# Kernel tuning notes

Measured on AMD Instinct MI355X. Metric: run time of the kernel, lower is better.

## Reference

```python
import jax, jax.numpy as jnp
import numpy as np

DIM = 1536
NHEADS = 12
HDIM = DIM // NHEADS  # 128
EPS = 1e-6
LOCAL_ATTN_SIZE = 3
SINK_SIZE = 1
MAX_ATTN = 32760 if LOCAL_ATTN_SIZE == -1 else LOCAL_ATTN_SIZE * 1560  # 4680


def _rms(x, g):
    # WanRMSNorm over last dim
    return x * jax.lax.rsqrt(jnp.mean(x * x, axis=-1, keepdims=True) + EPS) * g


def _rope(x, f, h, w, fr, fi, start_frame):
    # x: [b, s, n, d] with s == f*h*w; fr/fi: [1024, d//2] real/imag of complex rotations
    b, s, n, d = x.shape
    c = d // 2
    c0 = c - 2 * (c // 3)
    c1 = c // 3
    fc = jax.lax.complex(fr, fi)  # [1024, c]
    xr = x.reshape(b, s, n, c, 2)
    xc = jax.lax.complex(xr[..., 0], xr[..., 1])  # [b, s, n, c]
    ff = fc[start_frame:start_frame + f, :c0]      # [f, c0]
    fh = fc[:h, c0:c0 + c1]                        # [h, c1]
    fw = fc[:w, c0 + c1:c0 + 2 * c1]               # [w, c1]
    freqs_i = jnp.concatenate([
        jnp.broadcast_to(ff[:, None, None, :], (f, h, w, c0)),
        jnp.broadcast_to(fh[None, :, None, :], (f, h, w, c1)),
        jnp.broadcast_to(fw[None, None, :, :], (f, h, w, c1)),
    ], axis=-1).reshape(1, s, 1, c)
    y = xc * freqs_i
    return jnp.stack([y.real, y.imag], axis=-1).reshape(b, s, n, d)


def _attn(q, k, v):
    # plain SDPA (decode path of the module uses no mask on the gathered window)
    scale = 1.0 / np.sqrt(q.shape[-1]).astype(np.float32)
    logits = jnp.einsum('bqnd,bknd->bnqk', q, k) * scale
    p = jax.nn.softmax(logits, axis=-1)
    return jnp.einsum('bnqk,bknd->bqnd', p, v)


def _forward(x, cache_k, cache_v, freqs_real, freqs_imag,
             wq, bq, wk, bk, wv, bv, wo, bo, gq, gk,
             f_frames, height, width, current_start, global_end_index, local_end_index):
    b, s, _ = x.shape
    n, d = NHEADS, HDIM
    frame_seqlen = height * width
    start_frame = current_start // frame_seqlen

    q = _rms(x @ wq + bq, gq).reshape(b, s, n, d)
    k = _rms(x @ wk + bk, gk).reshape(b, s, n, d)
    v = (x @ wv + bv).reshape(b, s, n, d)

    rq = _rope(q, f_frames, height, width, freqs_real, freqs_imag, start_frame)
    rk = _rope(k, f_frames, height, width, freqs_real, freqs_imag, start_frame)

    current_end = current_start + s
    sink_tokens = SINK_SIZE * frame_seqlen
    kv_size = cache_k.shape[1]
    is_recompute = (current_end <= global_end_index) and (current_start > 0)

    kc, vc = cache_k, cache_v
    if LOCAL_ATTN_SIZE != -1 and current_end > global_end_index and s + local_end_index > kv_size:
        # evict oldest non-sink tokens, roll the rest toward the sink region
        num_evicted = s + local_end_index - kv_size
        num_rolled = local_end_index - num_evicted - sink_tokens
        src = slice(sink_tokens + num_evicted, sink_tokens + num_evicted + num_rolled)
        kc = kc.at[:, sink_tokens:sink_tokens + num_rolled].set(jax.lax.stop_gradient(cache_k[:, src]))
        vc = vc.at[:, sink_tokens:sink_tokens + num_rolled].set(jax.lax.stop_gradient(cache_v[:, src]))
        new_local_end = local_end_index + current_end - global_end_index - num_evicted
    else:
        new_local_end = local_end_index + current_end - global_end_index
    local_start = new_local_end - s
    write_start = max(local_start, sink_tokens) if is_recompute else local_start
    off = max(0, write_start - local_start)
    wl = max(0, new_local_end - write_start)
    if wl > 0:
        kc = kc.at[:, write_start:new_local_end].set(rk[:, off:off + wl])
        vc = vc.at[:, write_start:new_local_end].set(v[:, off:off + wl])

    if sink_tokens > 0:
        budget = MAX_ATTN - sink_tokens
        if budget > 0:
            lo = max(sink_tokens, new_local_end - budget)
            kcat = jnp.concatenate([kc[:, :sink_tokens], kc[:, lo:new_local_end]], axis=1)
            vcat = jnp.concatenate([vc[:, :sink_tokens], vc[:, lo:new_local_end]], axis=1)
        else:
            kcat, vcat = kc[:, :sink_tokens], vc[:, :sink_tokens]
        o = _attn(rq, kcat, vcat)
    else:
        ws = max(0, new_local_end - MAX_ATTN)
        o = _attn(rq, kc[:, ws:new_local_end], vc[:, ws:new_local_end])

    return o.reshape(b, s, DIM) @ wo + bo


def setup_inputs() -> dict:
    key = jax.random.key(0)
    ks = jax.random.split(key, 12)
    B, S, CACHE = 1, 1560, 4680
    sc = 0.02
    # RoPE tables as unit-magnitude complex rotations
    ang = jax.random.uniform(ks[0], (1024, HDIM // 2), jnp.float32, 0.0, 2.0 * np.pi)
    return {
        'x': jax.random.normal(ks[1], (B, S, DIM), jnp.float32),
        'cache_k': jax.random.normal(ks[2], (B, CACHE, NHEADS, HDIM), jnp.float32),
        'cache_v': jax.random.normal(ks[3], (B, CACHE, NHEADS, HDIM), jnp.float32),
        'freqs_real': jnp.cos(ang),
        'freqs_imag': jnp.sin(ang),
        'wq': jax.random.normal(ks[4], (DIM, DIM), jnp.float32) * sc,
        'bq': jnp.zeros((DIM,), jnp.float32),
        'wk': jax.random.normal(ks[5], (DIM, DIM), jnp.float32) * sc,
        'bk': jnp.zeros((DIM,), jnp.float32),
        'wv': jax.random.normal(ks[6], (DIM, DIM), jnp.float32) * sc,
        'bv': jnp.zeros((DIM,), jnp.float32),
        'wo': jax.random.normal(ks[7], (DIM, DIM), jnp.float32) * sc,
        'bo': jnp.zeros((DIM,), jnp.float32),
        'gq': jnp.ones((DIM,), jnp.float32),
        'gk': jnp.ones((DIM,), jnp.float32),
        'f_frames': 1,
        'height': 30,
        'width': 52,
        'current_start': 4680,
        'global_end_index': 4680,
        'local_end_index': 4680,
    }


def reference(x, cache_k, cache_v, freqs_real, freqs_imag,
              wq, bq, wk, bk, wv, bv, wo, bo, gq, gk,
              f_frames, height, width, current_start, global_end_index, local_end_index):
    return _forward(x, cache_k, cache_v, freqs_real, freqs_imag,
                    wq, bq, wk, bk, wv, bv, wo, bo, gq, gk,
                    f_frames, height, width, current_start, global_end_index, local_end_index)
```

## Files before the change

### kernel.cpp

```cpp
#include <hip/hip_runtime.h>
#include <cstdint>
#include <cstddef>

typedef unsigned int  u32;
typedef unsigned short u16;
typedef short s16x8 __attribute__((ext_vector_type(8)));
typedef float f32x4 __attribute__((ext_vector_type(4)));

#define DIM     1536
#define NH      12
#define HD      128
#define SEQ     1560
#define MPAD    1664
#define NKV     4680
#define NKPAD   4736
#define ROLL0   3120
#define NQK     4608
#define START_FRAME 3
#define NEGINF  -3.0e4f
#define NSPLIT  4
#define SPLITKC 1216

__device__ __forceinline__ u16 f2bf(float f){
  u32 u = __builtin_bit_cast(u32, f);
  u32 r = (u + 0x7fffu + ((u >> 16) & 1u)) >> 16;
  return (u16)r;
}

__global__ void k_pre(const float* __restrict__ x, u16* __restrict__ xp,
                      u16* __restrict__ Kc, u16* __restrict__ VT,
                      u16* __restrict__ Qr, u16* __restrict__ Opad,
                      float* __restrict__ sumsq,
                      const float* __restrict__ ck, const float* __restrict__ cv,
                      const float* __restrict__ wq, const float* __restrict__ wk,
                      const float* __restrict__ wv, const float* __restrict__ wo,
                      u16* __restrict__ WTqkv, u16* __restrict__ WTo){
  __shared__ u32 tile[64][65];
  int b = blockIdx.x, t = threadIdx.x;
  if (b < 244){
    int i = b * 256 + t;
    uint4 z = make_uint4(0u, 0u, 0u, 0u);
    if (i < 10752){
      int h = i / 896, r = i % 896;
      ((uint4*)(Kc + ((size_t)h * NKPAD + NKV) * 128))[r] = z;
    } else if (i < 21504){
      int j = i - 10752; int row = j / 7, c = j % 7;
      ((uint4*)(VT + (size_t)row * NKPAD + NKV))[c] = z;
    } else if (i < 41472){
      int j = i - 21504; int h = j / 1664, r = j % 1664;
      ((uint4*)(Qr + ((size_t)h * MPAD + SEQ) * 128))[r] = z;
    } else if (i < 61440){
      int r = i - 41472;
      ((uint4*)(Opad + (size_t)SEQ * DIM))[r] = z;
    } else if (i < 62272){
      ((uint4*)sumsq)[i - 61440] = z;
    }
  } else if (b < 1492){
    int i = (b - 244) * 256 + t;
    const int n_src = SEQ * DIM / 8;
    u16 o[8] = {0,0,0,0,0,0,0,0};
    if (i < n_src){
      float4 a = ((const float4*)x)[2*i];
      float4 c = ((const float4*)x)[2*i + 1];
      o[0]=f2bf(a.x); o[1]=f2bf(a.y); o[2]=f2bf(a.z); o[3]=f2bf(a.w);
      o[4]=f2bf(c.x); o[5]=f2bf(c.y); o[6]=f2bf(c.z); o[7]=f2bf(c.w);
    }
    uint4 v = make_uint4((u32)o[0]|((u32)o[1]<<16), (u32)o[2]|((u32)o[3]<<16),
                         (u32)o[4]|((u32)o[5]<<16), (u32)o[6]|((u32)o[7]<<16));
    ((uint4*)xp)[i] = v;
  } else if (b < 3832){
    int i = (b - 1492) * 256 + t;
    int p = i / 192, j = i - p * 192;
    int src = (p < SEQ) ? p : p + SEQ;
    int h = j >> 4, d = (j & 15) * 8;
    const float* s = ck + (size_t)src * DIM + j * 8;
    float4 a = ((const float4*)s)[0], bb = ((const float4*)s)[1];
    uint4 v = make_uint4((u32)f2bf(a.x)|((u32)f2bf(a.y)<<16), (u32)f2bf(a.z)|((u32)f2bf(a.w)<<16),
                         (u32)f2bf(bb.x)|((u32)f2bf(bb.y)<<16), (u32)f2bf(bb.z)|((u32)f2bf(bb.w)<<16));
    *(uint4*)(Kc + (size_t)(h * NKPAD + p) * 128 + d) = v;
  } else if (b < 5008){
    int idx = b - 3832;
    int p0 = (idx % 49) * 64, hd0 = (idx / 49) * 64;
    int pr = t >> 4, cg = t & 15;
#pragma unroll
    for (int i = 0; i < 4; i++){
      int p = p0 + pr + i * 16;
      if (p < ROLL0){
        int src = (p < SEQ) ? p : p + SEQ;
        float4 v = *(const float4*)(cv + (size_t)src * DIM + hd0 + cg * 4);
        tile[pr + i*16][cg*4+0] = f2bf(v.x); tile[pr + i*16][cg*4+1] = f2bf(v.y);
        tile[pr + i*16][cg*4+2] = f2bf(v.z); tile[pr + i*16][cg*4+3] = f2bf(v.w);
      }
    }
    __syncthreads();
    int hd = t >> 2, pg = t & 3;
    int pbase = p0 + pg * 16;
    if (pbase < ROLL0){
      u32 wds[8];
#pragma unroll
      for (int j = 0; j < 8; j++)
        wds[j] = (tile[pg*16 + 2*j][hd] & 0xffffu) | (tile[pg*16 + 2*j + 1][hd] << 16);
      u16* q = VT + (size_t)(hd0 + hd) * NKPAD + pbase;
      *(uint4*)q       = make_uint4(wds[0], wds[1], wds[2], wds[3]);
      *(uint4*)(q + 8) = make_uint4(wds[4], wds[5], wds[6], wds[7]);
    }
  } else {
    int idx = b - 5008;
    int z = idx / 576, rem = idx % 576;
    const float* w = (z==0)?wq:(z==1)?wk:(z==2)?wv:wo;
    u16* dst = (z < 3) ? (WTqkv + (size_t)z * DIM * DIM) : WTo;
    int r0 = (rem % 24) * 64, c0 = (rem / 24) * 64;
    int rr = t >> 4, cg = t & 15;
#pragma unroll
    for (int i = 0; i < 4; i++){
      int r = rr + i * 16;
      float4 v = *(const float4*)(w + (size_t)(r0 + r) * DIM + c0 + cg * 4);
      tile[r][cg*4+0] = f2bf(v.x); tile[r][cg*4+1] = f2bf(v.y);
      tile[r][cg*4+2] = f2bf(v.z); tile[r][cg*4+3] = f2bf(v.w);
    }
    __syncthreads();
    int c = t >> 2, rg = t & 3;
    u32 wds[8];
#pragma unroll
    for (int j = 0; j < 8; j++)
      wds[j] = (tile[rg*16 + 2*j][c] & 0xffffu) | (tile[rg*16 + 2*j + 1][c] << 16);
    u16* q = dst + (size_t)(c0 + c) * DIM + r0 + rg * 16;
    *(uint4*)q       = make_uint4(wds[0], wds[1], wds[2], wds[3]);
    *(uint4*)(q + 8) = make_uint4(wds[4], wds[5], wds[6], wds[7]);
  }
}

#define LDK 40
__global__ __launch_bounds__(512) void k_gemm_qkv(
    const u16* __restrict__ A, const u16* __restrict__ B,
    const float* __restrict__ biasq, const float* __restrict__ biask, const float* __restrict__ biasv,
    float* __restrict__ Y, float* __restrict__ sumsq, u16* __restrict__ VT){
  __shared__ u16 As[128*LDK];
  __shared__ u16 Bs[256*LDK];
  int orig = blockIdx.y * 18 + blockIdx.x;
  int xcd = orig & 7, jj = orig >> 3;
  int wg = (xcd < 2 ? xcd * 30 : 60 + (xcd - 2) * 29) + jj;
  int n0 = (wg % 18) * 256;
  int m0 = (wg / 18) * 128;
  int t = threadIdx.x, w = t >> 6, lane = t & 63, quad = lane >> 4, lc = lane & 15;
  int wm = w & 1, wn = w >> 1;
  int ar = t >> 2, ac = (t & 3) * 8;
  int br = t >> 1, bc = (t & 1) * 16;
  f32x4 acc[4][4] = {};
  uint4 pa, pb0, pb1;
  {
    pa = *(const uint4*)(A + (size_t)(m0 + ar) * DIM + ac);
    const uint4* gb = (const uint4*)(B + (size_t)(n0 + br) * DIM + bc);
    pb0 = gb[0]; pb1 = gb[1];
  }
  for (int kt = 0; kt < DIM/32; kt++){
    __syncthreads();
    *(uint4*)(As + ar * LDK + ac)     = pa;
    *(uint4*)(Bs + br * LDK + bc)     = pb0;
    *(uint4*)(Bs + br * LDK + bc + 8) = pb1;
    __syncthreads();
    if (kt + 1 < DIM/32){
      int k0 = (kt + 1) * 32;
      pa = *(const uint4*)(A + (size_t)(m0 + ar) * DIM + k0 + ac);
      const uint4* gb = (const uint4*)(B + (size_t)(n0 + br) * DIM + k0 + bc);
      pb0 = gb[0]; pb1 = gb[1];
    }
    s16x8 af[4], bf[4];
#pragma unroll
    for (int mt = 0; mt < 4; mt++) af[mt] = *(const s16x8*)(As + (wm*64 + mt*16 + lc) * LDK + quad * 8);
#pragma unroll
    for (int nt = 0; nt < 4; nt++) bf[nt] = *(const s16x8*)(Bs + (wn*64 + nt*16 + lc) * LDK + quad * 8);
#pragma unroll
    for (int mt = 0; mt < 4; mt++)
#pragma unroll
      for (int nt = 0; nt < 4; nt++)
        acc[mt][nt] = __builtin_amdgcn_mfma_f32_16x16x32_bf16(af[mt], bf[nt], acc[mt][nt], 0, 0, 0);
  }
  const float* bias; int cbase; int which;
  if (n0 < DIM)        { bias = biasq; cbase = 0;     which = 0; }
  else if (n0 < 2*DIM) { bias = biask; cbase = DIM;   which = 1; }
  else                 { bias = biasv; cbase = 2*DIM; which = 2; }
  float bvals[4];
#pragma unroll
  for (int nt = 0; nt < 4; nt++) bvals[nt] = bias[n0 - cbase + wn*64 + nt*16 + lc];
  if (which == 2){
#pragma unroll
    for (int mt = 0; mt < 4; mt++){
      int row0 = m0 + wm*64 + mt*16 + quad*4;
      if (row0 < SEQ){
#pragma unroll
        for (int nt = 0; nt < 4; nt++){
          int hd = (n0 - 2*DIM) + wn*64 + nt*16 + lc;
          u32 lo = (u32)f2bf(acc[mt][nt][0] + bvals[nt]) | ((u32)f2bf(acc[mt][nt][1] + bvals[nt]) << 16);
          u32 hi = (u32)f2bf(acc[mt][nt][2] + bvals[nt]) | ((u32)f2bf(acc[mt][nt][3] + bvals[nt]) << 16);
          *(uint2*)(VT + (size_t)hd * NKPAD + ROLL0 + row0) = make_uint2(lo, hi);
        }
      }
    }
  } else {
#pragma unroll
    for (int mt = 0; mt < 4; mt++){
      int row0 = m0 + wm*64 + mt*16 + quad*4;
      float ss[4] = {0.f, 0.f, 0.f, 0.f};
#pragma unroll
      for (int nt = 0; nt < 4; nt++){
        int col = n0 + wn*64 + nt*16 + lc;
#pragma unroll
        for (int r = 0; r < 4; r++){
          float y = acc[mt][nt][r] + bvals[nt];
          Y[(size_t)(row0 + r) * NQK + col] = y;
          ss[r] += y * y;
        }
      }
      float* dst = sumsq + (which ? MPAD : 0);
#pragma unroll
      for (int r = 0; r < 4; r++){
        float v = ss[r];
        v += __shfl_xor(v, 1); v += __shfl_xor(v, 2); v += __shfl_xor(v, 4); v += __shfl_xor(v, 8);
        if (lc == 0) atomicAdd(&dst[row0 + r], v);
      }
    }
  }
}

__global__ void k_rope_qk(const float* __restrict__ Y, const float* __restrict__ sumsq,
                          const float* __restrict__ gq, const float* __restrict__ gk,
                          const float* __restrict__ fre, const float* __restrict__ fim,
                          u16* __restrict__ Qr, u16* __restrict__ Kc){
  int pos = blockIdx.x;
  int t = threadIdx.x;
  float scq = rsqrtf(sumsq[pos]        * (1.0f/1536.0f) + 1e-6f);
  float sck = rsqrtf(sumsq[MPAD + pos] * (1.0f/1536.0f) + 1e-6f);
  int hrow = pos / 52, wrow = pos % 52;
#pragma unroll
  for (int i = 0; i < 3; i++){
    int p = t + i * 256;
    int head = p >> 6, j = p & 63;
    int frow = (j < 22) ? START_FRAME : ((j < 43) ? hrow : wrow);
    float cr = fre[frow * 64 + j], ci = fim[frow * 64 + j];
    int d0 = head * 128 + 2 * j;
    float2 yq = *(const float2*)(Y + (size_t)pos * NQK + d0);
    float qa = yq.x * scq * gq[d0];
    float qb = yq.y * scq * gq[d0 + 1];
    u32 oq = (u32)f2bf(qa * cr - qb * ci) | ((u32)f2bf(qa * ci + qb * cr) << 16);
    *(u32*)(Qr + (size_t)(head * MPAD + pos) * 128 + 2 * j) = oq;
    float2 yk = *(const float2*)(Y + (size_t)pos * NQK + DIM + d0);
    float ka = yk.x * sck * gk[d0];
    float kb = yk.y * sck * gk[d0 + 1];
    u32 ok = (u32)f2bf(ka * cr - kb * ci) | ((u32)f2bf(ka * ci + kb * cr) << 16);
    *(u32*)(Kc + (size_t)(head * NKPAD + ROLL0 + pos) * 128 + 2 * j) = ok;
  }
}

#define DEFER_THR 8.0f
__global__ __launch_bounds__(512, 4) void k_attn(const u16* __restrict__ Qr, const u16* __restrict__ Kc,
                                                 const u16* __restrict__ VT,
                                                 float* __restrict__ Opart, float* __restrict__ ml){
  __shared__ u16 Ks[64 * 128];
  __shared__ u16 Vs[128 * 64];
  int h = blockIdx.y, qb = blockIdx.x, sp = blockIdx.z;
  int t = threadIdx.x, w = t >> 6, lane = t & 63, quad = lane >> 4, lc = lane & 15;
  int qbase = qb * 128 + w * 16;
  const u16* Qbase = Qr + (size_t)(h * MPAD + qbase + lc) * 128;
  s16x8 qf[4];
#pragma unroll
  for (int kk = 0; kk < 4; kk++) qf[kk] = *(const s16x8*)(Qbase + kk * 32 + quad * 8);
  f32x4 oacc[8] = {};
  float m_ = NEGINF;
  float l_ = 0.f;
  const float scale = 0.08838834764831845f;
  const u16* Kh = Kc + (size_t)h * NKPAD * 128;
  const u16* Vh = VT + (size_t)h * 128 * NKPAD;
  int kr0 = t >> 4,          kg0 = (t & 15) * 8;
  int kr1 = (t + 512) >> 4,  kg1 = ((t + 512) & 15) * 8;
  int vd0 = t >> 3,          vp0 = (t & 7) * 8;
  int vd1 = (t + 512) >> 3,  vp1 = ((t + 512) & 7) * 8;
  int ksw0 = kr0 * 128 + (kg0 ^ ((kr0 & 7) << 3));
  int ksw1 = kr1 * 128 + (kg1 ^ ((kr1 & 7) << 3));
  int vsw0 = vd0 * 64  + (vp0 ^ ((vd0 & 7) << 3));
  int vsw1 = vd1 * 64  + (vp1 ^ ((vd1 & 7) << 3));
  int xork = (lc & 7) << 3;
  int aa = (lc + ((quad & 1) << 5)) << 2;
  int ab = aa + 64;
  int hi = quad >> 1;

  int kc0 = sp * SPLITKC;
  int kc1 = (sp == NSPLIT-1) ? NKPAD : kc0 + SPLITKC;
  uint4 kp0, kp1, vq0, vq1;
  {
    int kc = kc0;
    kp0 = *(const uint4*)(Kh + (size_t)(kc + kr0) * 128 + kg0);
    kp1 = *(const uint4*)(Kh + (size_t)(kc + kr1) * 128 + kg1);
    vq0 = *(const uint4*)(Vh + (size_t)vd0 * NKPAD + kc + vp0);
    vq1 = *(const uint4*)(Vh + (size_t)vd1 * NKPAD + kc + vp1);
  }
  for (int kc = kc0; kc < kc1; kc += 64){
    __syncthreads();
    *(uint4*)(Ks + ksw0) = kp0;
    *(uint4*)(Ks + ksw1) = kp1;
    *(uint4*)(Vs + vsw0) = vq0;
    *(uint4*)(Vs + vsw1) = vq1;
    __syncthreads();
    if (kc + 64 < kc1){
      int kn = kc + 64;
      kp0 = *(const uint4*)(Kh + (size_t)(kn + kr0) * 128 + kg0);
      kp1 = *(const uint4*)(Kh + (size_t)(kn + kr1) * 128 + kg1);
      vq0 = *(const uint4*)(Vh + (size_t)vd0 * NKPAD + kn + vp0);
      vq1 = *(const uint4*)(Vh + (size_t)vd1 * NKPAD + kn + vp1);
    }
    float s[4][4];
    __builtin_amdgcn_s_setprio(1);
#pragma unroll
    for (int nt = 0; nt < 4; nt++){
      f32x4 acc = {};
      int p = nt * 16 + lc;
#pragma unroll
      for (int kk = 0; kk < 4; kk++){
        s16x8 kf = *(const s16x8*)(Ks + p * 128 + (((kk * 4 + quad) * 8) ^ xork));
        acc = __builtin_amdgcn_mfma_f32_16x16x32_bf16(kf, qf[kk], acc, 0, 0, 0);
      }
#pragma unroll
      for (int r = 0; r < 4; r++) s[nt][r] = acc[r] * scale;
    }
    __builtin_amdgcn_s_setprio(0);
    if (kc + 64 > NKV){
#pragma unroll
      for (int nt = 0; nt < 4; nt++){
        int keyb = kc + nt * 16 + quad * 4;
#pragma unroll
        for (int r = 0; r < 4; r++) if (keyb + r >= NKV) s[nt][r] = NEGINF;
      }
    }
    float mx = fmaxf(fmaxf(s[0][0], s[0][1]), fmaxf(s[0][2], s[0][3]));
#pragma unroll
    for (int nt = 1; nt < 4; nt++)
      mx = fmaxf(mx, fmaxf(fmaxf(s[nt][0], s[nt][1]), fmaxf(s[nt][2], s[nt][3])));
    mx = fmaxf(mx, __shfl_xor(mx, 16));
    mx = fmaxf(mx, __shfl_xor(mx, 32));
    if (__any(mx > m_ + DEFER_THR)){
      float mnew = fmaxf(m_, mx);
      float alpha = __expf(m_ - mnew);
      m_ = mnew; l_ *= alpha;
      float alr[4];
#pragma unroll
      for (int r = 0; r < 4; r++) alr[r] = __shfl(alpha, quad * 4 + r);
#pragma unroll
      for (int dt = 0; dt < 8; dt++){
        f32x4 oo = oacc[dt];
#pragma unroll
        for (int r = 0; r < 4; r++) oo[r] *= alr[r];
        oacc[dt] = oo;
      }
    }
#pragma unroll
    for (int nt = 0; nt < 4; nt++)
#pragma unroll
      for (int r = 0; r < 4; r++) s[nt][r] = __expf(s[nt][r] - m_);
    float sum = (s[0][0] + s[0][1]) + (s[0][2] + s[0][3]);
#pragma unroll
    for (int nt = 1; nt < 4; nt++)
      sum += (s[nt][0] + s[nt][1]) + (s[nt][2] + s[nt][3]);
    sum += __shfl_xor(sum, 16);
    sum += __shfl_xor(sum, 32);
    l_ += sum;
    u32 w01[4], w23[4];
#pragma unroll
    for (int nt = 0; nt < 4; nt++){
      w01[nt] = (u32)f2bf(s[nt][0]) | ((u32)f2bf(s[nt][1]) << 16);
      w23[nt] = (u32)f2bf(s[nt][2]) | ((u32)f2bf(s[nt][3]) << 16);
    }
    u32 x0, x1;
    uint4 A0, A1;
    x0 = (u32)__builtin_amdgcn_ds_bpermute(aa, (int)w01[0]);
    x1 = (u32)__builtin_amdgcn_ds_bpermute(aa, (int)w01[1]);
    A0.x = hi ? x1 : x0;
    x0 = (u32)__builtin_amdgcn_ds_bpermute(aa, (int)w23[0]);
    x1 = (u32)__builtin_amdgcn_ds_bpermute(aa, (int)w23[1]);
    A0.y = hi ? x1 : x0;
    x0 = (u32)__builtin_amdgcn_ds_bpermute(ab, (int)w01[0]);
    x1 = (u32)__builtin_amdgcn_ds_bpermute(ab, (int)w01[1]);
    A0.z = hi ? x1 : x0;
    x0 = (u32)__builtin_amdgcn_ds_bpermute(ab, (int)w23[0]);
    x1 = (u32)__builtin_amdgcn_ds_bpermute(ab, (int)w23[1]);
    A0.w = hi ? x1 : x0;
    x0 = (u32)__builtin_amdgcn_ds_bpermute(aa, (int)w01[2]);
    x1 = (u32)__builtin_amdgcn_ds_bpermute(aa, (int)w01[3]);
    A1.x = hi ? x1 : x0;
    x0 = (u32)__builtin_amdgcn_ds_bpermute(aa, (int)w23[2]);
    x1 = (u32)__builtin_amdgcn_ds_bpermute(aa, (int)w23[3]);
    A1.y = hi ? x1 : x0;
    x0 = (u32)__builtin_amdgcn_ds_bpermute(ab, (int)w01[2]);
    x1 = (u32)__builtin_amdgcn_ds_bpermute(ab, (int)w01[3]);
    A1.z = hi ? x1 : x0;
    x0 = (u32)__builtin_amdgcn_ds_bpermute(ab, (int)w23[2]);
    x1 = (u32)__builtin_amdgcn_ds_bpermute(ab, (int)w23[3]);
    A1.w = hi ? x1 : x0;
    s16x8 a0 = __builtin_bit_cast(s16x8, A0);
    s16x8 a1 = __builtin_bit_cast(s16x8, A1);
    __builtin_amdgcn_s_setprio(1);
#pragma unroll
    for (int dt = 0; dt < 8; dt++){
      int d = dt * 16 + lc;
      s16x8 v0 = *(const s16x8*)(Vs + d * 64 + ((quad * 8) ^ xork));
      s16x8 v1 = *(const s16x8*)(Vs + d * 64 + ((32 + quad * 8) ^ xork));
      oacc[dt] = __builtin_amdgcn_mfma_f32_16x16x32_bf16(a0, v0, oacc[dt], 0, 0, 0);
      oacc[dt] = __builtin_amdgcn_mfma_f32_16x16x32_bf16(a1, v1, oacc[dt], 0, 0, 0);
    }
    __builtin_amdgcn_s_setprio(0);
  }
  float mr[4], lr[4];
#pragma unroll
  for (int r = 0; r < 4; r++){
    mr[r] = __shfl(m_, quad * 4 + r);
    lr[r] = __shfl(l_, quad * 4 + r);
  }
  float* Ob = Opart + ((size_t)(sp * NH + h) * SEQ) * 128;
  float* mlb = ml + ((size_t)(sp * NH + h) * SEQ) * 2;
#pragma unroll
  for (int dt = 0; dt < 8; dt++)
#pragma unroll
    for (int r = 0; r < 4; r++){
      int row = qbase + quad * 4 + r;
      if (row < SEQ) Ob[(size_t)row * 128 + dt * 16 + lc] = oacc[dt][r];
    }
  if (lc == 0){
#pragma unroll
    for (int r = 0; r < 4; r++){
      int row = qbase + quad * 4 + r;
      if (row < SEQ){
        mlb[row * 2 + 0] = mr[r];
        mlb[row * 2 + 1] = lr[r];
      }
    }
  }
}

__global__ void k_attn_cmb(const float* __restrict__ Opart, const float* __restrict__ ml,
                           u16* __restrict__ Og){
  int row = blockIdx.x, h = blockIdx.y, d = threadIdx.x;
  float m[NSPLIT], l[NSPLIT];
  float M = NEGINF;
#pragma unroll
  for (int s = 0; s < NSPLIT; s++){
    m[s] = ml[((size_t)(s * NH + h) * SEQ + row) * 2 + 0];
    l[s] = ml[((size_t)(s * NH + h) * SEQ + row) * 2 + 1];
    M = fmaxf(M, m[s]);
  }
  float L = 0.f, o = 0.f;
#pragma unroll
  for (int s = 0; s < NSPLIT; s++){
    float wgt = __expf(m[s] - M);
    L += wgt * l[s];
    o += wgt * Opart[((size_t)(s * NH + h) * SEQ + row) * 128 + d];
  }
  Og[(size_t)row * DIM + h * 128 + d] = f2bf(o / L);
}

__global__ __launch_bounds__(256) void k_gemm_out(const u16* __restrict__ A, const u16* __restrict__ B,
                                                  const float* __restrict__ bo, float* __restrict__ out){
  __shared__ u16 As[128*LDK];
  __shared__ u16 Bs[128*LDK];
  int m0 = blockIdx.y * 128, n0 = blockIdx.x * 128;
  int t = threadIdx.x, w = t >> 6, lane = t & 63, quad = lane >> 4, lc = lane & 15;
  int wm = w & 1, wn = w >> 1;
  int sr = t >> 1, sh = (t & 1) * 16;
  f32x4 acc[4][4] = {};
  uint4 pa0, pa1, pb0, pb1;
  {
    const uint4* ga = (const uint4*)(A + (size_t)(m0 + sr) * DIM + sh);
    const uint4* gb = (const uint4*)(B + (size_t)(n0 + sr) * DIM + sh);
    pa0 = ga[0]; pa1 = ga[1]; pb0 = gb[0]; pb1 = gb[1];
  }
  for (int kt = 0; kt < DIM/32; kt++){
    __syncthreads();
    *(uint4*)(As + sr * LDK + sh)     = pa0;
    *(uint4*)(As + sr * LDK + sh + 8) = pa1;
    *(uint4*)(Bs + sr * LDK + sh)     = pb0;
    *(uint4*)(Bs + sr * LDK + sh + 8) = pb1;
    __syncthreads();
    if (kt + 1 < DIM/32){
      int k0 = (kt + 1) * 32;
      const uint4* ga = (const uint4*)(A + (size_t)(m0 + sr) * DIM + k0 + sh);
      const uint4* gb = (const uint4*)(B + (size_t)(n0 + sr) * DIM + k0 + sh);
      pa0 = ga[0]; pa1 = ga[1]; pb0 = gb[0]; pb1 = gb[1];
    }
    s16x8 af[4], bf[4];
#pragma unroll
    for (int mt = 0; mt < 4; mt++) af[mt] = *(const s16x8*)(As + (wm*64 + mt*16 + lc) * LDK + quad * 8);
#pragma unroll
    for (int nt = 0; nt < 4; nt++) bf[nt] = *(const s16x8*)(Bs + (wn*64 + nt*16 + lc) * LDK + quad * 8);
#pragma unroll
    for (int mt = 0; mt < 4; mt++)
#pragma unroll
      for (int nt = 0; nt < 4; nt++)
        acc[mt][nt] = __builtin_amdgcn_mfma_f32_16x16x32_bf16(af[mt], bf[nt], acc[mt][nt], 0, 0, 0);
  }
  float bvals[4];
#pragma unroll
  for (int nt = 0; nt < 4; nt++) bvals[nt] = bo[n0 + wn*64 + nt*16 + lc];
#pragma unroll
  for (int mt = 0; mt < 4; mt++){
    int row0 = m0 + wm*64 + mt*16 + quad*4;
#pragma unroll
    for (int nt = 0; nt < 4; nt++){
      int col = n0 + wn*64 + nt*16 + lc;
#pragma unroll
      for (int r = 0; r < 4; r++){
        int row = row0 + r;
        if (row < SEQ) out[(size_t)row * DIM + col] = acc[mt][nt][r] + bvals[nt];
      }
    }
  }
}

extern "C" void kernel_launch(void* const* d_in, const int* in_sizes, int n_in,
                              void* d_out, int out_size, void* d_ws, size_t ws_size,
                              hipStream_t stream){
  const float* x   = (const float*)d_in[0];
  const float* ck  = (const float*)d_in[1];
  const float* cv  = (const float*)d_in[2];
  const float* fre = (const float*)d_in[3];
  const float* fim = (const float*)d_in[4];
  const float* wq  = (const float*)d_in[5];
  const float* bq  = (const float*)d_in[6];
  const float* wk  = (const float*)d_in[7];
  const float* bk  = (const float*)d_in[8];
  const float* wv  = (const float*)d_in[9];
  const float* bv  = (const float*)d_in[10];
  const float* wo  = (const float*)d_in[11];
  const float* bo  = (const float*)d_in[12];
  const float* gq  = (const float*)d_in[13];
  const float* gk  = (const float*)d_in[14];

  char* ws = (char*)d_ws;
  size_t off = 0;
  u16*   xpad  = (u16*)(ws + off);  off += (size_t)MPAD * DIM * 2;
  u16*   WTqkv = (u16*)(ws + off);  off += (size_t)3 * DIM * DIM * 2;
  float* Y     = (float*)(ws + off); off += (size_t)MPAD * NQK * 4;
  u16*   WTo   = (u16*)(ws + off);  off += (size_t)DIM * DIM * 2;
  float* sumsq = (float*)(ws + off); off += (size_t)2 * MPAD * 4;
  u16*   Qr    = (u16*)(ws + off);  off += (size_t)NH * MPAD * 128 * 2;
  u16*   Kc    = (u16*)(ws + off);  off += (size_t)NH * NKPAD * 128 * 2;
  u16*   VT    = (u16*)(ws + off);  off += (size_t)NH * 128 * NKPAD * 2;
  u16*   Opad  = (u16*)(ws + off);  off += (size_t)MPAD * DIM * 2;
  if (off > ws_size) return;
  float* Opart = (float*)ws;
  float* ml    = (float*)(ws + (size_t)NSPLIT * NH * SEQ * 128 * 4);

  k_pre         <<<dim3(7312), 256, 0, stream>>>(x, xpad, Kc, VT, Qr, Opad, sumsq, ck, cv,
                                                 wq, wk, wv, wo, WTqkv, WTo);
  k_gemm_qkv    <<<dim3(18, 13), 512, 0, stream>>>(xpad, WTqkv, bq, bk, bv, Y, sumsq, VT);
  k_rope_qk     <<<dim3(SEQ), 256, 0, stream>>>(Y, sumsq, gq, gk, fre, fim, Qr, Kc);
  k_attn        <<<dim3(MPAD/128, NH, NSPLIT), 512, 0, stream>>>(Qr, Kc, VT, Opart, ml);
  k_attn_cmb    <<<dim3(SEQ, NH), 128, 0, stream>>>(Opart, ml, Opad);
  k_gemm_out    <<<dim3(DIM/128, MPAD/128), 256, 0, stream>>>(Opad, WTo, bo, (float*)d_out);
}
```

Baseline: 355.8 us.

## Fuse split-K attention combine into attention kernel via last-block atomic counter

Removes the separate combine kernel launch. Each attention block bumps a per-(query block, head) atomic counter after writing its partial output, and the last split block to arrive merges all partials into the bf16 output with float4 loads. This saves one launch and its scheduling gap, and lets the combine overlap with other attention blocks still running. In exchange it adds threadfences and an atomic per block, leaves the combine to only 156 blocks, and relies on the counters being zeroed in the pre kernel on every call.

```diff
diff --git a/kernel.cpp b/kernel.cpp
--- a/kernel.cpp
+++ b/kernel.cpp
@@ -30,7 +30,7 @@
 __global__ void k_pre(const float* __restrict__ x, u16* __restrict__ xp,
                       u16* __restrict__ Kc, u16* __restrict__ VT,
                       u16* __restrict__ Qr, u16* __restrict__ Opad,
-                      float* __restrict__ sumsq,
+                      float* __restrict__ sumsq, int* __restrict__ cnt,
                       const float* __restrict__ ck, const float* __restrict__ cv,
                       const float* __restrict__ wq, const float* __restrict__ wk,
                       const float* __restrict__ wv, const float* __restrict__ wo,
@@ -54,6 +54,8 @@
       ((uint4*)(Opad + (size_t)SEQ * DIM))[r] = z;
     } else if (i < 62272){
       ((uint4*)sumsq)[i - 61440] = z;
+    } else if (i < 62311){
+      ((uint4*)cnt)[i - 62272] = z;
     }
   } else if (b < 1492){
     int i = (b - 244) * 256 + t;
@@ -255,9 +257,11 @@
 #define DEFER_THR 8.0f
 __global__ __launch_bounds__(512, 4) void k_attn(const u16* __restrict__ Qr, const u16* __restrict__ Kc,
                                                  const u16* __restrict__ VT,
-                                                 float* __restrict__ Opart, float* __restrict__ ml){
+                                                 float* __restrict__ Opart, float* __restrict__ ml,
+                                                 u16* __restrict__ Og, int* __restrict__ cnt){
   __shared__ u16 Ks[64 * 128];
   __shared__ u16 Vs[128 * 64];
+  __shared__ int lastFlag;
   int h = blockIdx.y, qb = blockIdx.x, sp = blockIdx.z;
   int t = threadIdx.x, w = t >> 6, lane = t & 63, quad = lane >> 4, lc = lane & 15;
   int qbase = qb * 128 + w * 16;
@@ -282,7 +286,7 @@
   int xork = (lc & 7) << 3;
   int aa = (lc + ((quad & 1) << 5)) << 2;
   int ab = aa + 64;
-  int hi = quad >> 1;
+  int hw2 = quad >> 1;
 
   int kc0 = sp * SPLITKC;
   int kc1 = (sp == NSPLIT-1) ? NKPAD : kc0 + SPLITKC;
@@ -373,28 +377,28 @@
     uint4 A0, A1;
     x0 = (u32)__builtin_amdgcn_ds_bpermute(aa, (int)w01[0]);
     x1 = (u32)__builtin_amdgcn_ds_bpermute(aa, (int)w01[1]);
-    A0.x = hi ? x1 : x0;
+    A0.x = hw2 ? x1 : x0;
     x0 = (u32)__builtin_amdgcn_ds_bpermute(aa, (int)w23[0]);
     x1 = (u32)__builtin_amdgcn_ds_bpermute(aa, (int)w23[1]);
-    A0.y = hi ? x1 : x0;
+    A0.y = hw2 ? x1 : x0;
     x0 = (u32)__builtin_amdgcn_ds_bpermute(ab, (int)w01[0]);
     x1 = (u32)__builtin_amdgcn_ds_bpermute(ab, (int)w01[1]);
-    A0.z = hi ? x1 : x0;
+    A0.z = hw2 ? x1 : x0;
     x0 = (u32)__builtin_amdgcn_ds_bpermute(ab, (int)w23[0]);
     x1 = (u32)__builtin_amdgcn_ds_bpermute(ab, (int)w23[1]);
-    A0.w = hi ? x1 : x0;
+    A0.w = hw2 ? x1 : x0;
     x0 = (u32)__builtin_amdgcn_ds_bpermute(aa, (int)w01[2]);
     x1 = (u32)__builtin_amdgcn_ds_bpermute(aa, (int)w01[3]);
-    A1.x = hi ? x1 : x0;
+    A1.x = hw2 ? x1 : x0;
     x0 = (u32)__builtin_amdgcn_ds_bpermute(aa, (int)w23[2]);
     x1 = (u32)__builtin_amdgcn_ds_bpermute(aa, (int)w23[3]);
-    A1.y = hi ? x1 : x0;
+    A1.y = hw2 ? x1 : x0;
     x0 = (u32)__builtin_amdgcn_ds_bpermute(ab, (int)w01[2]);
     x1 = (u32)__builtin_amdgcn_ds_bpermute(ab, (int)w01[3]);
-    A1.z = hi ? x1 : x0;
+    A1.z = hw2 ? x1 : x0;
     x0 = (u32)__builtin_amdgcn_ds_bpermute(ab, (int)w23[2]);
     x1 = (u32)__builtin_amdgcn_ds_bpermute(ab, (int)w23[3]);
-    A1.w = hi ? x1 : x0;
+    A1.w = hw2 ? x1 : x0;
     s16x8 a0 = __builtin_bit_cast(s16x8, A0);
     s16x8 a1 = __builtin_bit_cast(s16x8, A1);
     __builtin_amdgcn_s_setprio(1);
@@ -433,27 +437,38 @@
       }
     }
   }
-}
-
-__global__ void k_attn_cmb(const float* __restrict__ Opart, const float* __restrict__ ml,
-                           u16* __restrict__ Og){
-  int row = blockIdx.x, h = blockIdx.y, d = threadIdx.x;
-  float m[NSPLIT], l[NSPLIT];
-  float M = NEGINF;
-#pragma unroll
-  for (int s = 0; s < NSPLIT; s++){
-    m[s] = ml[((size_t)(s * NH + h) * SEQ + row) * 2 + 0];
-    l[s] = ml[((size_t)(s * NH + h) * SEQ + row) * 2 + 1];
-    M = fmaxf(M, m[s]);
-  }
-  float L = 0.f, o = 0.f;
-#pragma unroll
-  for (int s = 0; s < NSPLIT; s++){
-    float wgt = __expf(m[s] - M);
-    L += wgt * l[s];
-    o += wgt * Opart[((size_t)(s * NH + h) * SEQ + row) * 128 + d];
-  }
-  Og[(size_t)row * DIM + h * 128 + d] = f2bf(o / L);
+  __threadfence();
+  __syncthreads();
+  if (t == 0) lastFlag = (atomicAdd(&cnt[qb * NH + h], 1) == NSPLIT - 1);
+  __syncthreads();
+  if (!lastFlag) return;
+  __threadfence();
+  for (int i = t; i < 128 * 32; i += 512){
+    int row = qb * 128 + (i >> 5);
+    if (row >= SEQ) continue;
+    int d4 = (i & 31) << 2;
+    float mm[NSPLIT], llv[NSPLIT];
+    float M = NEGINF;
+#pragma unroll
+    for (int s2 = 0; s2 < NSPLIT; s2++){
+      mm[s2]  = ml[((size_t)(s2 * NH + h) * SEQ + row) * 2 + 0];
+      llv[s2] = ml[((size_t)(s2 * NH + h) * SEQ + row) * 2 + 1];
+      M = fmaxf(M, mm[s2]);
+    }
+    float L = 0.f;
+    float ox = 0.f, oy = 0.f, oz = 0.f, ow = 0.f;
+#pragma unroll
+    for (int s2 = 0; s2 < NSPLIT; s2++){
+      float wgt = __expf(mm[s2] - M);
+      L += wgt * llv[s2];
+      float4 op = *(const float4*)(Opart + ((size_t)(s2 * NH + h) * SEQ + row) * 128 + d4);
+      ox += wgt * op.x; oy += wgt * op.y; oz += wgt * op.z; ow += wgt * op.w;
+    }
+    float inv = 1.0f / L;
+    u32 lo  = (u32)f2bf(ox * inv) | ((u32)f2bf(oy * inv) << 16);
+    u32 hi2 = (u32)f2bf(oz * inv) | ((u32)f2bf(ow * inv) << 16);
+    *(uint2*)(Og + (size_t)row * DIM + h * 128 + d4) = make_uint2(lo, hi2);
+  }
 }
 
 __global__ __launch_bounds__(256) void k_gemm_out(const u16* __restrict__ A, const u16* __restrict__ B,
@@ -539,6 +554,7 @@
   float* Y     = (float*)(ws + off); off += (size_t)MPAD * NQK * 4;
   u16*   WTo   = (u16*)(ws + off);  off += (size_t)DIM * DIM * 2;
   float* sumsq = (float*)(ws + off); off += (size_t)2 * MPAD * 4;
+  int*   cnt   = (int*)(ws + off);  off += (size_t)39 * 16;
   u16*   Qr    = (u16*)(ws + off);  off += (size_t)NH * MPAD * 128 * 2;
   u16*   Kc    = (u16*)(ws + off);  off += (size_t)NH * NKPAD * 128 * 2;
   u16*   VT    = (u16*)(ws + off);  off += (size_t)NH * 128 * NKPAD * 2;
@@ -547,11 +563,10 @@
   float* Opart = (float*)ws;
   float* ml    = (float*)(ws + (size_t)NSPLIT * NH * SEQ * 128 * 4);
 
-  k_pre         <<<dim3(7312), 256, 0, stream>>>(x, xpad, Kc, VT, Qr, Opad, sumsq, ck, cv,
+  k_pre         <<<dim3(7312), 256, 0, stream>>>(x, xpad, Kc, VT, Qr, Opad, sumsq, cnt, ck, cv,
                                                  wq, wk, wv, wo, WTqkv, WTo);
   k_gemm_qkv    <<<dim3(18, 13), 512, 0, stream>>>(xpad, WTqkv, bq, bk, bv, Y, sumsq, VT);
   k_rope_qk     <<<dim3(SEQ), 256, 0, stream>>>(Y, sumsq, gq, gk, fre, fim, Qr, Kc);
-  k_attn        <<<dim3(MPAD/128, NH, NSPLIT), 512, 0, stream>>>(Qr, Kc, VT, Opart, ml);
-  k_attn_cmb    <<<dim3(SEQ, NH), 128, 0, stream>>>(Opart, ml, Opad);
+  k_attn        <<<dim3(MPAD/128, NH, NSPLIT), 512, 0, stream>>>(Qr, Kc, VT, Opart, ml, Opad, cnt);
   k_gemm_out    <<<dim3(DIM/128, MPAD/128), 256, 0, stream>>>(Opad, WTo, bo, (float*)d_out);
 }
```

New measurement: 552.5 us. 55.3% more time.
